# Performance work log

Hardware: AMD Instinct MI355X
Metric: run time of the kernel (lower is better)

## Reference

```python
import jax, jax.numpy as jnp
import numpy as np
from jax import lax

M, T, D, E, NTAGS = 512, 512, 128, 512, 74
GH = D // 2   # GRU hidden per direction (64)
LH = E // 2   # LSTM hidden per direction (256)


def _gru_dir(x, Wih, Whh, bih, bhh):
    # x: [T, Din] -> [T, H]; PyTorch gate order r, z, n
    h = Whh.shape[1]
    gi = x @ Wih.T + bih  # [T, 3H] precomputed input projections
    def step(hprev, gi_t):
        gh = hprev @ Whh.T + bhh
        r = jax.nn.sigmoid(gi_t[:h] + gh[:h])
        z = jax.nn.sigmoid(gi_t[h:2 * h] + gh[h:2 * h])
        n = jnp.tanh(gi_t[2 * h:] + r * gh[2 * h:])
        hnew = (1.0 - z) * n + z * hprev
        return hnew, hnew
    _, hs = lax.scan(step, jnp.zeros((h,), x.dtype), gi)
    return hs


def _bigru(x, Wf, Uf, bf, cf, Wb, Ub, bb, cb):
    hf = _gru_dir(x, Wf, Uf, bf, cf)
    hb = _gru_dir(x[::-1], Wb, Ub, bb, cb)[::-1]
    return jnp.concatenate([hf, hb], axis=-1)


def _lstm_dir(x, Wih, Whh, bih, bhh):
    # PyTorch gate order i, f, g, o
    h = Whh.shape[1]
    gi = x @ Wih.T + bih  # [T, 4H]
    def step(carry, gi_t):
        hprev, cprev = carry
        g = gi_t + hprev @ Whh.T + bhh
        i = jax.nn.sigmoid(g[:h])
        f = jax.nn.sigmoid(g[h:2 * h])
        gg = jnp.tanh(g[2 * h:3 * h])
        o = jax.nn.sigmoid(g[3 * h:])
        c = f * cprev + i * gg
        hnew = o * jnp.tanh(c)
        return (hnew, c), hnew
    init = (jnp.zeros((h,), x.dtype), jnp.zeros((h,), x.dtype))
    _, hs = lax.scan(step, init, gi)
    return hs


def _bilstm(x, Wf, Uf, bf, cf, Wb, Ub, bb, cb):
    hf = _lstm_dir(x, Wf, Uf, bf, cf)
    hb = _lstm_dir(x[::-1], Wb, Ub, bb, cb)[::-1]
    return jnp.concatenate([hf, hb], axis=-1)


def setup_inputs() -> dict:
    key = jax.random.key(0)
    ks = jax.random.split(key, 32)
    s = 0.05
    def n(k, shape, scale=s):
        return jax.random.normal(k, shape, jnp.float32) * scale
    inp = {
        'memory': jax.random.normal(ks[0], (M, T, D), jnp.float32),
        'u': jax.random.normal(ks[1], (T, D), jnp.float32),
        'embed': jax.random.normal(ks[2], (T, E), jnp.float32),
        'W_ff': n(ks[3], (D, 2 * D)), 'b_ff': n(ks[4], (D,)),
        'gWih_f': n(ks[5], (3 * GH, D)), 'gWhh_f': n(ks[6], (3 * GH, GH)),
        'gbih_f': n(ks[7], (3 * GH,)), 'gbhh_f': n(ks[8], (3 * GH,)),
        'gWih_b': n(ks[9], (3 * GH, D)), 'gWhh_b': n(ks[10], (3 * GH, GH)),
        'gbih_b': n(ks[11], (3 * GH,)), 'gbhh_b': n(ks[12], (3 * GH,)),
        'W_k': n(ks[13], (E, D)), 'b_k': n(ks[14], (E,)),
        'lWih_f': n(ks[15], (4 * LH, E)), 'lWhh_f': n(ks[16], (4 * LH, LH)),
        'lbih_f': n(ks[17], (4 * LH,)), 'lbhh_f': n(ks[18], (4 * LH,)),
        'lWih_b': n(ks[19], (4 * LH, E)), 'lWhh_b': n(ks[20], (4 * LH, LH)),
        'lbih_b': n(ks[21], (4 * LH,)), 'lbhh_b': n(ks[22], (4 * LH,)),
        'W_out': n(ks[23], (NTAGS, E)), 'b_out': n(ks[24], (NTAGS,)),
    }
    return inp


def reference(memory, u, embed, W_ff, b_ff,
              gWih_f, gWhh_f, gbih_f, gbhh_f,
              gWih_b, gWhh_b, gbih_b, gbhh_b,
              W_k, b_k,
              lWih_f, lWhh_f, lbih_f, lbhh_f,
              lWih_b, lWhh_b, lbih_b, lbhh_b,
              W_out, b_out):
    # --- memory attention (original: python loop over self._memory) ---
    # p[i] = <flatten(memory[i]), flatten(u)>; softmax over memories
    p = jax.nn.softmax(jnp.einsum('mtd,td->m', memory, u))  # [M]
    cat = jnp.concatenate([memory, jnp.broadcast_to(u, memory.shape)], axis=-1)  # [M,T,2D]
    g = cat @ W_ff.T + b_ff  # [M,T,D] (ff_layer applied per memory)
    G = jnp.einsum('m,mtd->td', p, g)  # weighted sum over memories [T,D]
    # --- session encoder (bidirectional GRU) ---
    h = _bigru(G, gWih_f, gWhh_f, gbih_f, gbhh_f, gWib := gWih_b, gWhh_b, gbih_b, gbhh_b)  # [T,D]
    # --- knowledge encoder ---
    o = (u + h) @ W_k.T + b_k  # [T,E]
    # --- tagging head: BiLSTM over embed + o, then linear + softmax ---
    x = embed + o
    comb = _bilstm(x, lWih_f, lWhh_f, lbih_f, lbhh_f, lWih_b, lWhh_b, lbih_b, lbhh_b)  # [T,E]
    logits = comb @ W_out.T + b_out  # [T, NTAGS]
    return jax.nn.softmax(logits, axis=-1)
```

## Files before the change

### kernel.cpp

```cpp
#include <hip/hip_runtime.h>
#include <math.h>

#define TT 512
#define DD 128
#define MM 512
#define EE 512
#define NTAGS 74
#define GH 64
#define LH 256

typedef _Float16 half_t;
typedef _Float16 v2h __attribute__((ext_vector_type(2)));
typedef _Float16 v8h __attribute__((ext_vector_type(8)));
typedef _Float16 v16h __attribute__((ext_vector_type(16)));
typedef int v4i __attribute__((ext_vector_type(4)));

__device__ __forceinline__ float fdot2f(v2h a, v2h b, float c) {
#if __has_builtin(__builtin_amdgcn_fdot2)
    return __builtin_amdgcn_fdot2(a, b, c, false);
#else
    return c + (float)a[0] * (float)b[0] + (float)a[1] * (float)b[1];
#endif
}

__device__ __forceinline__ int sdot4(int a, int b, int c) {
#if __has_builtin(__builtin_amdgcn_sdot4)
    return __builtin_amdgcn_sdot4(a, b, c, false);
#else
    return c + ((a << 24) >> 24) * ((b << 24) >> 24)
             + ((a << 16) >> 24) * ((b << 16) >> 24)
             + ((a << 8) >> 24) * ((b << 8) >> 24)
             + (a >> 24) * (b >> 24);
#endif
}

__device__ __forceinline__ float sigf(float x) { return 1.f / (1.f + __expf(-x)); }
__device__ __forceinline__ float tanhfast(float x) { return 1.f - 2.f / (__expf(2.f * x) + 1.f); }

__device__ __forceinline__ void lds_barrier() {
    __builtin_amdgcn_sched_barrier(0);
    asm volatile("s_waitcnt lgkmcnt(0)" ::: "memory");
    __builtin_amdgcn_s_barrier();
    __builtin_amdgcn_sched_barrier(0);
}

__device__ __forceinline__ v16h load16(const float* p) {
    float4 x0 = ((const float4*)p)[0];
    float4 x1 = ((const float4*)p)[1];
    float4 x2 = ((const float4*)p)[2];
    float4 x3 = ((const float4*)p)[3];
    v16h r;
    r[0] = (half_t)x0.x; r[1] = (half_t)x0.y; r[2] = (half_t)x0.z; r[3] = (half_t)x0.w;
    r[4] = (half_t)x1.x; r[5] = (half_t)x1.y; r[6] = (half_t)x1.z; r[7] = (half_t)x1.w;
    r[8] = (half_t)x2.x; r[9] = (half_t)x2.y; r[10] = (half_t)x2.z; r[11] = (half_t)x2.w;
    r[12] = (half_t)x3.x; r[13] = (half_t)x3.y; r[14] = (half_t)x3.z; r[15] = (half_t)x3.w;
    return r;
}

#define OPAQUE4(a, b, c, d) \
    asm volatile("" : "+v"(a), "+v"(b), "+v"(c), "+v"(d))
#define OPAQUE6(a, b, c, d, e, f) \
    asm volatile("" : "+v"(a), "+v"(b), "+v"(c), "+v"(d), "+v"(e), "+v"(f))

__device__ __forceinline__ void dot16(const v16h& w, const v8h& h0, const v8h& h1,
                                      float& x0, float& x1) {
    x0 = fdot2f(v2h{w[0], w[1]}, v2h{h0[0], h0[1]}, x0);
    x1 = fdot2f(v2h{w[2], w[3]}, v2h{h0[2], h0[3]}, x1);
    x0 = fdot2f(v2h{w[4], w[5]}, v2h{h0[4], h0[5]}, x0);
    x1 = fdot2f(v2h{w[6], w[7]}, v2h{h0[6], h0[7]}, x1);
    x0 = fdot2f(v2h{w[8], w[9]}, v2h{h1[0], h1[1]}, x0);
    x1 = fdot2f(v2h{w[10], w[11]}, v2h{h1[2], h1[3]}, x1);
    x0 = fdot2f(v2h{w[12], w[13]}, v2h{h1[4], h1[5]}, x0);
    x1 = fdot2f(v2h{w[14], w[15]}, v2h{h1[6], h1[7]}, x1);
}

__device__ __forceinline__ int pack4(int b0, int b1, int b2, int b3) {
    return (b0 & 0xff) | ((b1 & 0xff) << 8) | ((b2 & 0xff) << 16) | (b3 << 24);
}

__device__ __forceinline__ v4i quant16(const float* p, float inv_s) {
    float4 x0 = ((const float4*)p)[0];
    float4 x1 = ((const float4*)p)[1];
    float4 x2 = ((const float4*)p)[2];
    float4 x3 = ((const float4*)p)[3];
    v4i r;
    r.x = pack4(__float2int_rn(x0.x * inv_s), __float2int_rn(x0.y * inv_s),
                __float2int_rn(x0.z * inv_s), __float2int_rn(x0.w * inv_s));
    r.y = pack4(__float2int_rn(x1.x * inv_s), __float2int_rn(x1.y * inv_s),
                __float2int_rn(x1.z * inv_s), __float2int_rn(x1.w * inv_s));
    r.z = pack4(__float2int_rn(x2.x * inv_s), __float2int_rn(x2.y * inv_s),
                __float2int_rn(x2.z * inv_s), __float2int_rn(x2.w * inv_s));
    r.w = pack4(__float2int_rn(x3.x * inv_s), __float2int_rn(x3.y * inv_s),
                __float2int_rn(x3.z * inv_s), __float2int_rn(x3.w * inv_s));
    return r;
}

__global__ __launch_bounds__(256) void k_dots(const float* __restrict__ mem,
                                              const float* __restrict__ u,
                                              float* __restrict__ dots) {
    int m = blockIdx.x;
    const float4* m4 = (const float4*)(mem + (size_t)m * TT * DD);
    const float4* u4 = (const float4*)u;
    float acc = 0.f;
#pragma unroll 4
    for (int it = 0; it < (TT * DD / 4) / 256; ++it) {
        int i = it * 256 + threadIdx.x;
        float4 a = m4[i], b = u4[i];
        acc += a.x * b.x + a.y * b.y + a.z * b.z + a.w * b.w;
    }
    for (int off = 32; off; off >>= 1) acc += __shfl_down(acc, off, 64);
    __shared__ float red[4];
    int w = threadIdx.x >> 6, l = threadIdx.x & 63;
    if (l == 0) red[w] = acc;
    __syncthreads();
    if (threadIdx.x == 0) dots[m] = red[0] + red[1] + red[2] + red[3];
}

__global__ __launch_bounds__(512) void k_softmax_p(const float* __restrict__ dots,
                                                   float* __restrict__ p) {
    int tid = threadIdx.x;
    float v = dots[tid];
    float mx = v;
    for (int off = 32; off; off >>= 1) mx = fmaxf(mx, __shfl_down(mx, off, 64));
    __shared__ float red[8];
    __shared__ float bm, bs;
    int w = tid >> 6, l = tid & 63;
    if (l == 0) red[w] = mx;
    __syncthreads();
    if (tid == 0) {
        float t = red[0];
        for (int i = 1; i < 8; ++i) t = fmaxf(t, red[i]);
        bm = t;
    }
    __syncthreads();
    float e = __expf(v - bm);
    float sm = e;
    for (int off = 32; off; off >>= 1) sm += __shfl_down(sm, off, 64);
    if (l == 0) red[w] = sm;
    __syncthreads();
    if (tid == 0) {
        float t = 0.f;
        for (int i = 0; i < 8; ++i) t += red[i];
        bs = t;
    }
    __syncthreads();
    p[tid] = e / bs;
}

__global__ __launch_bounds__(128) void k_wsum(const float* __restrict__ mem,
                                              const float* __restrict__ p,
                                              float* __restrict__ Mbar) {
    __shared__ float pl[MM];
    for (int i = threadIdx.x; i < MM; i += 128) pl[i] = p[i];
    __syncthreads();
    int i4 = blockIdx.x * 128 + threadIdx.x;
    const float4* m4 = (const float4*)mem;
    float4 acc = {0.f, 0.f, 0.f, 0.f};
#pragma unroll 4
    for (int m = 0; m < MM; ++m) {
        float pm = pl[m];
        float4 a = m4[(size_t)m * (TT * DD / 4) + i4];
        acc.x += pm * a.x; acc.y += pm * a.y; acc.z += pm * a.z; acc.w += pm * a.w;
    }
    ((float4*)Mbar)[i4] = acc;
}

__global__ __launch_bounds__(128) void k_G(const float* __restrict__ Mbar,
                                           const float* __restrict__ u,
                                           const float* __restrict__ Wff,
                                           const float* __restrict__ bff,
                                           float* __restrict__ G) {
    int t = blockIdx.x, d = threadIdx.x;
    __shared__ __align__(16) float Ml[DD], ul[DD];
    Ml[d] = Mbar[t * DD + d];
    ul[d] = u[t * DD + d];
    __syncthreads();
    const float* wr = Wff + (size_t)d * 2 * DD;
    float a0 = 0.f, a1 = 0.f;
#pragma unroll 4
    for (int k = 0; k < DD; ++k) {
        a0 += Ml[k] * wr[k];
        a1 += ul[k] * wr[DD + k];
    }
    G[t * DD + d] = a0 + a1 + bff[d];
}

__global__ __launch_bounds__(384) void k_gru_gi(const float* __restrict__ G,
                                                const float* __restrict__ Wf,
                                                const float* __restrict__ bf,
                                                const float* __restrict__ Wb,
                                                const float* __restrict__ bb,
                                                float* __restrict__ gi) {
    int t = blockIdx.x;
    __shared__ __align__(16) float Gl[DD];
    if (threadIdx.x < DD) Gl[threadIdx.x] = G[t * DD + threadIdx.x];
    __syncthreads();
    int r = threadIdx.x;
    const float* w;
    float b;
    float* o;
    if (r < 192) {
        w = Wf + (size_t)r * DD; b = bf[r]; o = gi + ((size_t)0 * TT + t) * 192 + r;
    } else {
        int rr = r - 192;
        w = Wb + (size_t)rr * DD; b = bb[rr]; o = gi + ((size_t)1 * TT + t) * 192 + rr;
    }
    float a0 = 0.f, a1 = 0.f;
#pragma unroll 4
    for (int k = 0; k < DD; k += 2) {
        a0 += Gl[k] * w[k];
        a1 += Gl[k + 1] * w[k + 1];
    }
    *o = a0 + a1 + b;
}

__global__ __launch_bounds__(256) void k_gru_seq(const float* __restrict__ Whh_f,
                                                 const float* __restrict__ bhh_f,
                                                 const float* __restrict__ Whh_b,
                                                 const float* __restrict__ bhh_b,
                                                 const float* __restrict__ gi,
                                                 float* __restrict__ hbuf) {
    int dir = blockIdx.x;
    int tid = threadIdx.x;
    const float* Whh = dir ? Whh_b : Whh_f;
    const float* bhh = dir ? bhh_b : bhh_f;
    v16h w0 = {}, w1 = {}, w2 = {}, w3 = {};
    float bh = 0.f;
    if (tid < 192) {
        const float* wr = Whh + (size_t)tid * 64;
        w0 = load16(wr);
        w1 = load16(wr + 16);
        w2 = load16(wr + 32);
        w3 = load16(wr + 48);
        bh = bhh[tid];
    }
    OPAQUE4(w0, w1, w2, w3);
    __shared__ __align__(16) half_t hl[64];
    __shared__ float pa[192];
    if (tid < 32) ((v2h*)hl)[tid] = v2h{(half_t)0.f, (half_t)0.f};
    float h = 0.f;
    float g_r = 0.f, g_z = 0.f, g_n = 0.f;
    if (tid < 64) {
        int t0 = dir ? (TT - 1) : 0;
        const float* git = gi + ((size_t)dir * TT + t0) * 192;
        g_r = git[tid]; g_z = git[64 + tid]; g_n = git[128 + tid];
    }
    lds_barrier();
    for (int s = 0; s < TT; ++s) {
        int t = dir ? (TT - 1 - s) : s;
        float p_r = 0.f, p_z = 0.f, p_n = 0.f;
        if (tid < 64) {
            int sn = (s + 1 < TT) ? (s + 1) : s;
            int tn = dir ? (TT - 1 - sn) : sn;
            const float* git = gi + ((size_t)dir * TT + tn) * 192;
            p_r = git[tid]; p_z = git[64 + tid]; p_n = git[128 + tid];
        }
        if (tid < 192) {
            float a0 = bh, a1 = 0.f;
            v8h h0, h1;
            h0 = *(const v8h*)(hl + 0);  h1 = *(const v8h*)(hl + 8);
            dot16(w0, h0, h1, a0, a1);
            h0 = *(const v8h*)(hl + 16); h1 = *(const v8h*)(hl + 24);
            dot16(w1, h0, h1, a0, a1);
            h0 = *(const v8h*)(hl + 32); h1 = *(const v8h*)(hl + 40);
            dot16(w2, h0, h1, a0, a1);
            h0 = *(const v8h*)(hl + 48); h1 = *(const v8h*)(hl + 56);
            dot16(w3, h0, h1, a0, a1);
            pa[tid] = a0 + a1;
        }
        lds_barrier();
        if (tid < 64) {
            float r = sigf(g_r + pa[tid]);
            float z = sigf(g_z + pa[64 + tid]);
            float n = tanhfast(g_n + r * pa[128 + tid]);
            h = (1.f - z) * n + z * h;
            hbuf[t * DD + dir * 64 + tid] = h;
            hl[tid] = (half_t)h;
        }
        lds_barrier();
        g_r = p_r; g_z = p_z; g_n = p_n;
    }
}

__global__ __launch_bounds__(512) void k_x(const float* __restrict__ u,
                                           const float* __restrict__ hbuf,
                                           const float* __restrict__ Wk,
                                           const float* __restrict__ bk,
                                           const float* __restrict__ embed,
                                           float* __restrict__ x) {
    int t = blockIdx.x, e = threadIdx.x;
    __shared__ __align__(16) float sl[DD];
    if (e < DD) sl[e] = u[t * DD + e] + hbuf[t * DD + e];
    __syncthreads();
    const float* wr = Wk + (size_t)e * DD;
    float a0 = 0.f, a1 = 0.f;
#pragma unroll 4
    for (int k = 0; k < DD; k += 2) {
        a0 += sl[k] * wr[k];
        a1 += sl[k + 1] * wr[k + 1];
    }
    x[t * EE + e] = embed[t * EE + e] + a0 + a1 + bk[e];
}

__global__ __launch_bounds__(1024) void k_lstm_gi(const float* __restrict__ x,
                                                  const float* __restrict__ Wf,
                                                  const float* __restrict__ bf,
                                                  const float* __restrict__ Wb,
                                                  const float* __restrict__ bb,
                                                  float* __restrict__ gi) {
    int dir = blockIdx.y;
    int t0 = blockIdx.x * 8;
    __shared__ __align__(16) float xl[8 * EE];
    for (int i = threadIdx.x; i < 8 * EE; i += 1024) xl[i] = x[(size_t)t0 * EE + i];
    __syncthreads();
    int r = threadIdx.x;
    const float* W = dir ? Wb : Wf;
    const float* bi = dir ? bb : bf;
    const float* wr = W + (size_t)r * EE;
    float b = bi[r];
    float acc[8];
#pragma unroll
    for (int uu = 0; uu < 8; ++uu) acc[uu] = b;
    for (int k = 0; k < EE; k += 4) {
        float4 wv = *(const float4*)(wr + k);
#pragma unroll
        for (int uu = 0; uu < 8; ++uu) {
            float4 xv = *(const float4*)(&xl[uu * EE + k]);
            acc[uu] += wv.x * xv.x + wv.y * xv.y + wv.z * xv.z + wv.w * xv.w;
        }
    }
#pragma unroll
    for (int uu = 0; uu < 8; ++uu)
        gi[((size_t)dir * TT + (t0 + uu)) * 1024 + r] = acc[uu];
}

__global__ __launch_bounds__(512) void k_lstm_seq(const float* __restrict__ Whh_f,
                                                  const float* __restrict__ bhh_f,
                                                  const float* __restrict__ Whh_b,
                                                  const float* __restrict__ bhh_b,
                                                  const float* __restrict__ gi,
                                                  float* __restrict__ comb) {
    int dir = blockIdx.x;
    int tid = threadIdx.x;
    int u = tid & 255;
    int hi = tid >> 8;
    int r0 = hi * 256 + u;
    int r1 = 512 + hi * 256 + u;
    const float* Whh = dir ? Whh_b : Whh_f;
    const float* bhh = dir ? bhh_b : bhh_f;

    __shared__ __align__(16) int wsl[4][1024][4];
    __shared__ __align__(16) int hq[64];
    __shared__ float pa[1024];

    const float* s0 = Whh + (size_t)r0 * 256;
    const float* s1 = Whh + (size_t)r1 * 256;
    float mx0 = 0.f, mx1 = 0.f;
    for (int k = 0; k < 256; k += 4) {
        float4 a = *(const float4*)(s0 + k);
        float4 b = *(const float4*)(s1 + k);
        mx0 = fmaxf(mx0, fmaxf(fmaxf(fabsf(a.x), fabsf(a.y)), fmaxf(fabsf(a.z), fabsf(a.w))));
        mx1 = fmaxf(mx1, fmaxf(fmaxf(fabsf(b.x), fabsf(b.y)), fmaxf(fabsf(b.z), fabsf(b.w))));
    }
    float inv0 = 127.f / mx0, inv1 = 127.f / mx1;
    float fs0 = mx0 / 16129.f, fs1 = mx1 / 16129.f;

#pragma unroll
    for (int cc = 0; cc < 4; ++cc) {
        *(v4i*)&wsl[cc][r0][0] = quant16(s0 + 192 + 16 * cc, inv0);
        *(v4i*)&wsl[cc][r1][0] = quant16(s1 + 192 + 16 * cc, inv1);
    }
    v4i wa0 = quant16(s0, inv0),        wa1 = quant16(s0 + 16, inv0),
        wa2 = quant16(s0 + 32, inv0),   wa3 = quant16(s0 + 48, inv0),
        wa4 = quant16(s0 + 64, inv0),   wa5 = quant16(s0 + 80, inv0),
        wa6 = quant16(s0 + 96, inv0),   wa7 = quant16(s0 + 112, inv0),
        wa8 = quant16(s0 + 128, inv0),  wa9 = quant16(s0 + 144, inv0),
        wa10 = quant16(s0 + 160, inv0), wa11 = quant16(s0 + 176, inv0);
    v4i wb0 = quant16(s1, inv1),        wb1 = quant16(s1 + 16, inv1),
        wb2 = quant16(s1 + 32, inv1),   wb3 = quant16(s1 + 48, inv1),
        wb4 = quant16(s1 + 64, inv1),   wb5 = quant16(s1 + 80, inv1),
        wb6 = quant16(s1 + 96, inv1),   wb7 = quant16(s1 + 112, inv1),
        wb8 = quant16(s1 + 128, inv1),  wb9 = quant16(s1 + 144, inv1),
        wb10 = quant16(s1 + 160, inv1), wb11 = quant16(s1 + 176, inv1);
    OPAQUE6(wa0, wa1, wa2, wa3, wa4, wa5);
    OPAQUE6(wa6, wa7, wa8, wa9, wa10, wa11);
    OPAQUE6(wb0, wb1, wb2, wb3, wb4, wb5);
    OPAQUE6(wb6, wb7, wb8, wb9, wb10, wb11);
    float bh0 = bhh[r0], bh1 = bhh[r1];
    if (tid < 64) hq[tid] = 0;
    float c_state = 0.f;
    int tfirst = dir ? (TT - 1) : 0;
    float g0v = gi[((size_t)dir * TT + tfirst) * 1024 + r0];
    float g1v = gi[((size_t)dir * TT + tfirst) * 1024 + r1];
    lds_barrier();

    for (int s = 0; s < TT; ++s) {
        int t = dir ? (TT - 1 - s) : s;
        int sn = (s + 1 < TT) ? (s + 1) : s;
        int tn = dir ? (TT - 1 - sn) : sn;
        const float* gnext = gi + ((size_t)dir * TT + tn) * 1024;
        float g0n = gnext[r0], g1n = gnext[r1];
        int a0 = 0, a1 = 0, b0 = 0, b1 = 0;
        const v4i* h4 = (const v4i*)hq;
#define DOTC(c) { v4i h = h4[c];                                     \
        a0 = sdot4(wa##c.x, h.x, a0); a1 = sdot4(wa##c.y, h.y, a1);  \
        a0 = sdot4(wa##c.z, h.z, a0); a1 = sdot4(wa##c.w, h.w, a1);  \
        b0 = sdot4(wb##c.x, h.x, b0); b1 = sdot4(wb##c.y, h.y, b1);  \
        b0 = sdot4(wb##c.z, h.z, b0); b1 = sdot4(wb##c.w, h.w, b1); }
        DOTC(0); DOTC(1); DOTC(2); DOTC(3); DOTC(4); DOTC(5);
        DOTC(6); DOTC(7); DOTC(8); DOTC(9); DOTC(10); DOTC(11);
#undef DOTC
#pragma unroll
        for (int cc = 0; cc < 4; ++cc) {
            v4i h = h4[12 + cc];
            v4i va = *(const v4i*)&wsl[cc][r0][0];
            v4i vb = *(const v4i*)&wsl[cc][r1][0];
            a0 = sdot4(va.x, h.x, a0); a1 = sdot4(va.y, h.y, a1);
            a0 = sdot4(va.z, h.z, a0); a1 = sdot4(va.w, h.w, a1);
            b0 = sdot4(vb.x, h.x, b0); b1 = sdot4(vb.y, h.y, b1);
            b0 = sdot4(vb.z, h.z, b0); b1 = sdot4(vb.w, h.w, b1);
        }
        pa[r0] = (float)(a0 + a1) * fs0 + bh0 + g0v;
        pa[r1] = (float)(b0 + b1) * fs1 + bh1 + g1v;
        lds_barrier();
        if (tid < 256) {
            float iv = sigf(pa[tid]);
            float fv = sigf(pa[256 + tid]);
            float gv = tanhfast(pa[512 + tid]);
            float ov = sigf(pa[768 + tid]);
            c_state = fv * c_state + iv * gv;
            float h = ov * tanhfast(c_state);
            comb[(size_t)t * EE + dir * 256 + tid] = h;
            ((signed char*)hq)[tid] = (signed char)__float2int_rn(h * 127.f);
        }
        lds_barrier();
        g0v = g0n; g1v = g1n;
    }
}

__global__ __launch_bounds__(128) void k_out(const float* __restrict__ comb,
                                             const float* __restrict__ Wout,
                                             const float* __restrict__ bout,
                                             float* __restrict__ out) {
    int t = blockIdx.x;
    __shared__ __align__(16) float cl[EE];
    __shared__ float ll[NTAGS];
    __shared__ float mred, sred;
    for (int i = threadIdx.x; i < EE; i += 128) cl[i] = comb[(size_t)t * EE + i];
    __syncthreads();
    int e = threadIdx.x;
    if (e < NTAGS) {
        const float* wr = Wout + (size_t)e * EE;
        float a0 = 0.f, a1 = 0.f;
#pragma unroll 4
        for (int k = 0; k < EE; k += 2) {
            a0 += cl[k] * wr[k];
            a1 += cl[k + 1] * wr[k + 1];
        }
        ll[e] = a0 + a1 + bout[e];
    }
    __syncthreads();
    if (threadIdx.x == 0) {
        float m = ll[0];
        for (int i = 1; i < NTAGS; ++i) m = fmaxf(m, ll[i]);
        float ss = 0.f;
        for (int i = 0; i < NTAGS; ++i) ss += __expf(ll[i] - m);
        mred = m;
        sred = ss;
    }
    __syncthreads();
    if (e < NTAGS) out[t * NTAGS + e] = __expf(ll[e] - mred) / sred;
}

#define OFF_DOTS  ((size_t)0)
#define OFF_P     ((size_t)512)
#define OFF_MBAR  ((size_t)1024)
#define OFF_G     ((size_t)66560)
#define OFF_GIG   ((size_t)132096)
#define OFF_HBUF  ((size_t)328704)
#define OFF_X     ((size_t)394240)
#define OFF_GIL   ((size_t)656384)
#define OFF_COMB  ((size_t)1704960)

extern "C" void kernel_launch(void* const* d_in, const int* in_sizes, int n_in,
                              void* d_out, int out_size, void* d_ws, size_t ws_size,
                              hipStream_t stream) {
    const float* memory = (const float*)d_in[0];
    const float* u      = (const float*)d_in[1];
    const float* embed  = (const float*)d_in[2];
    const float* W_ff   = (const float*)d_in[3];
    const float* b_ff   = (const float*)d_in[4];
    const float* gWih_f = (const float*)d_in[5];
    const float* gWhh_f = (const float*)d_in[6];
    const float* gbih_f = (const float*)d_in[7];
    const float* gbhh_f = (const float*)d_in[8];
    const float* gWih_b = (const float*)d_in[9];
    const float* gWhh_b = (const float*)d_in[10];
    const float* gbih_b = (const float*)d_in[11];
    const float* gbhh_b = (const float*)d_in[12];
    const float* W_k    = (const float*)d_in[13];
    const float* b_k    = (const float*)d_in[14];
    const float* lWih_f = (const float*)d_in[15];
    const float* lWhh_f = (const float*)d_in[16];
    const float* lbih_f = (const float*)d_in[17];
    const float* lbhh_f = (const float*)d_in[18];
    const float* lWih_b = (const float*)d_in[19];
    const float* lWhh_b = (const float*)d_in[20];
    const float* lbih_b = (const float*)d_in[21];
    const float* lbhh_b = (const float*)d_in[22];
    const float* W_out  = (const float*)d_in[23];
    const float* b_out  = (const float*)d_in[24];
    float* out = (float*)d_out;
    float* ws = (float*)d_ws;

    float* dots = ws + OFF_DOTS;
    float* p    = ws + OFF_P;
    float* Mbar = ws + OFF_MBAR;
    float* G    = ws + OFF_G;
    float* giG  = ws + OFF_GIG;
    float* hbuf = ws + OFF_HBUF;
    float* x    = ws + OFF_X;
    float* giL  = ws + OFF_GIL;
    float* comb = ws + OFF_COMB;

    k_dots<<<MM, 256, 0, stream>>>(memory, u, dots);
    k_softmax_p<<<1, MM, 0, stream>>>(dots, p);
    k_wsum<<<128, 128, 0, stream>>>(memory, p, Mbar);
    k_G<<<TT, DD, 0, stream>>>(Mbar, u, W_ff, b_ff, G);
    k_gru_gi<<<TT, 384, 0, stream>>>(G, gWih_f, gbih_f, gWih_b, gbih_b, giG);
    k_gru_seq<<<2, 256, 0, stream>>>(gWhh_f, gbhh_f, gWhh_b, gbhh_b, giG, hbuf);
    k_x<<<TT, EE, 0, stream>>>(u, hbuf, W_k, b_k, embed, x);
    k_lstm_gi<<<dim3(64, 2), 1024, 0, stream>>>(x, lWih_f, lbih_f, lWih_b, lbih_b, giL);
    k_lstm_seq<<<2, 512, 0, stream>>>(lWhh_f, lbhh_f, lWhh_b, lbhh_b, giL, comb);
    k_out<<<TT, 128, 0, stream>>>(comb, W_out, b_out, out);
}
```

Measured before the change: 1.343 ms.

## Restructure GRU and LSTM recurrences to keep all gates per thread

The GRU recurrence now runs as a single 64-thread wavefront per direction. Each lane holds all three gate rows of its hidden unit, so the block barriers and the LDS partial-sum exchange become one wave-local LDS fence. The LSTM recurrence now gives each hidden unit a pair of lanes that split the K dimension, hold all four int8-quantized gate rows in registers, and combine partials with a shuffle. This removes the LDS weight spill, the pa buffer and one of the two block barriers per step, and double-buffers the quantized hidden state. The cost is heavier per-thread register and ALU work for each step.

After: 1.332 ms. Within noise of the previous version (-0.8%).

```diff
diff --git a/kernel.cpp b/kernel.cpp
--- a/kernel.cpp
+++ b/kernel.cpp
@@ -41,6 +41,12 @@
     __builtin_amdgcn_sched_barrier(0);
     asm volatile("s_waitcnt lgkmcnt(0)" ::: "memory");
     __builtin_amdgcn_s_barrier();
+    __builtin_amdgcn_sched_barrier(0);
+}
+
+__device__ __forceinline__ void wave_lds_fence() {
+    __builtin_amdgcn_sched_barrier(0);
+    asm volatile("s_waitcnt lgkmcnt(0)" ::: "memory");
     __builtin_amdgcn_sched_barrier(0);
 }
 
@@ -59,8 +65,6 @@
 
 #define OPAQUE4(a, b, c, d) \
     asm volatile("" : "+v"(a), "+v"(b), "+v"(c), "+v"(d))
-#define OPAQUE6(a, b, c, d, e, f) \
-    asm volatile("" : "+v"(a), "+v"(b), "+v"(c), "+v"(d), "+v"(e), "+v"(f))
 
 __device__ __forceinline__ void dot16(const v16h& w, const v8h& h0, const v8h& h1,
                                       float& x0, float& x1) {
@@ -95,6 +99,16 @@
     return r;
 }
 
+__device__ __forceinline__ float rowmax128(const float* p) {
+    float m = 0.f;
+#pragma unroll 8
+    for (int k = 0; k < 128; k += 4) {
+        float4 a = *(const float4*)(p + k);
+        m = fmaxf(m, fmaxf(fmaxf(fabsf(a.x), fabsf(a.y)), fmaxf(fabsf(a.z), fabsf(a.w))));
+    }
+    return m;
+}
+
 __global__ __launch_bounds__(256) void k_dots(const float* __restrict__ mem,
                                               const float* __restrict__ u,
                                               float* __restrict__ dots) {
@@ -214,71 +228,61 @@
     *o = a0 + a1 + b;
 }
 
-__global__ __launch_bounds__(256) void k_gru_seq(const float* __restrict__ Whh_f,
-                                                 const float* __restrict__ bhh_f,
-                                                 const float* __restrict__ Whh_b,
-                                                 const float* __restrict__ bhh_b,
-                                                 const float* __restrict__ gi,
-                                                 float* __restrict__ hbuf) {
+__global__ __launch_bounds__(64) void k_gru_seq(const float* __restrict__ Whh_f,
+                                                const float* __restrict__ bhh_f,
+                                                const float* __restrict__ Whh_b,
+                                                const float* __restrict__ bhh_b,
+                                                const float* __restrict__ gi,
+                                                float* __restrict__ hbuf) {
     int dir = blockIdx.x;
-    int tid = threadIdx.x;
+    int u = threadIdx.x;
     const float* Whh = dir ? Whh_b : Whh_f;
     const float* bhh = dir ? bhh_b : bhh_f;
-    v16h w0 = {}, w1 = {}, w2 = {}, w3 = {};
-    float bh = 0.f;
-    if (tid < 192) {
-        const float* wr = Whh + (size_t)tid * 64;
-        w0 = load16(wr);
-        w1 = load16(wr + 16);
-        w2 = load16(wr + 32);
-        w3 = load16(wr + 48);
-        bh = bhh[tid];
-    }
-    OPAQUE4(w0, w1, w2, w3);
+    const float* wr_ = Whh + (size_t)u * 64;
+    const float* wz_ = Whh + (size_t)(64 + u) * 64;
+    const float* wn_ = Whh + (size_t)(128 + u) * 64;
+    v16h wr0 = load16(wr_), wr1 = load16(wr_ + 16), wr2 = load16(wr_ + 32), wr3 = load16(wr_ + 48);
+    v16h wz0 = load16(wz_), wz1 = load16(wz_ + 16), wz2 = load16(wz_ + 32), wz3 = load16(wz_ + 48);
+    v16h wn0 = load16(wn_), wn1 = load16(wn_ + 16), wn2 = load16(wn_ + 32), wn3 = load16(wn_ + 48);
+    OPAQUE4(wr0, wr1, wr2, wr3);
+    OPAQUE4(wz0, wz1, wz2, wz3);
+    OPAQUE4(wn0, wn1, wn2, wn3);
+    float bh_r = bhh[u], bh_z = bhh[64 + u], bh_n = bhh[128 + u];
+
     __shared__ __align__(16) half_t hl[64];
-    __shared__ float pa[192];
-    if (tid < 32) ((v2h*)hl)[tid] = v2h{(half_t)0.f, (half_t)0.f};
+    hl[u] = (half_t)0.f;
     float h = 0.f;
-    float g_r = 0.f, g_z = 0.f, g_n = 0.f;
-    if (tid < 64) {
-        int t0 = dir ? (TT - 1) : 0;
-        const float* git = gi + ((size_t)dir * TT + t0) * 192;
-        g_r = git[tid]; g_z = git[64 + tid]; g_n = git[128 + tid];
-    }
-    lds_barrier();
+    int t0 = dir ? (TT - 1) : 0;
+    const float* g0p = gi + ((size_t)dir * TT + t0) * 192;
+    float g_r = g0p[u], g_z = g0p[64 + u], g_n = g0p[128 + u];
+    wave_lds_fence();
+
     for (int s = 0; s < TT; ++s) {
         int t = dir ? (TT - 1 - s) : s;
-        float p_r = 0.f, p_z = 0.f, p_n = 0.f;
-        if (tid < 64) {
-            int sn = (s + 1 < TT) ? (s + 1) : s;
-            int tn = dir ? (TT - 1 - sn) : sn;
-            const float* git = gi + ((size_t)dir * TT + tn) * 192;
-            p_r = git[tid]; p_z = git[64 + tid]; p_n = git[128 + tid];
-        }
-        if (tid < 192) {
-            float a0 = bh, a1 = 0.f;
-            v8h h0, h1;
-            h0 = *(const v8h*)(hl + 0);  h1 = *(const v8h*)(hl + 8);
-            dot16(w0, h0, h1, a0, a1);
-            h0 = *(const v8h*)(hl + 16); h1 = *(const v8h*)(hl + 24);
-            dot16(w1, h0, h1, a0, a1);
-            h0 = *(const v8h*)(hl + 32); h1 = *(const v8h*)(hl + 40);
-            dot16(w2, h0, h1, a0, a1);
-            h0 = *(const v8h*)(hl + 48); h1 = *(const v8h*)(hl + 56);
-            dot16(w3, h0, h1, a0, a1);
-            pa[tid] = a0 + a1;
-        }
-        lds_barrier();
-        if (tid < 64) {
-            float r = sigf(g_r + pa[tid]);
-            float z = sigf(g_z + pa[64 + tid]);
-            float n = tanhfast(g_n + r * pa[128 + tid]);
-            h = (1.f - z) * n + z * h;
-            hbuf[t * DD + dir * 64 + tid] = h;
-            hl[tid] = (half_t)h;
-        }
-        lds_barrier();
-        g_r = p_r; g_z = p_z; g_n = p_n;
+        int sn = (s + 1 < TT) ? (s + 1) : s;
+        int tn = dir ? (TT - 1 - sn) : sn;
+        const float* gb = gi + ((size_t)dir * TT + tn) * 192;
+        float pn_r = gb[u], pn_z = gb[64 + u], pn_n = gb[128 + u];
+
+        const v8h* hv = (const v8h*)hl;
+        v8h h0 = hv[0], h1 = hv[1], h2 = hv[2], h3 = hv[3];
+        v8h h4 = hv[4], h5 = hv[5], h6 = hv[6], h7 = hv[7];
+        float ar0 = bh_r, ar1 = 0.f, az0 = bh_z, az1 = 0.f, an0 = bh_n, an1 = 0.f;
+        dot16(wr0, h0, h1, ar0, ar1); dot16(wr1, h2, h3, ar0, ar1);
+        dot16(wr2, h4, h5, ar0, ar1); dot16(wr3, h6, h7, ar0, ar1);
+        dot16(wz0, h0, h1, az0, az1); dot16(wz1, h2, h3, az0, az1);
+        dot16(wz2, h4, h5, az0, az1); dot16(wz3, h6, h7, az0, az1);
+        dot16(wn0, h0, h1, an0, an1); dot16(wn1, h2, h3, an0, an1);
+        dot16(wn2, h4, h5, an0, an1); dot16(wn3, h6, h7, an0, an1);
+
+        float r = sigf(g_r + ar0 + ar1);
+        float z = sigf(g_z + az0 + az1);
+        float n = tanhfast(g_n + r * (an0 + an1));
+        h = (1.f - z) * n + z * h;
+        hbuf[t * DD + dir * 64 + u] = h;
+        hl[u] = (half_t)h;
+        wave_lds_fence();
+        g_r = pn_r; g_z = pn_z; g_n = pn_n;
     }
 }
 
@@ -334,108 +338,98 @@
         gi[((size_t)dir * TT + (t0 + uu)) * 1024 + r] = acc[uu];
 }
 
-__global__ __launch_bounds__(512) void k_lstm_seq(const float* __restrict__ Whh_f,
-                                                  const float* __restrict__ bhh_f,
-                                                  const float* __restrict__ Whh_b,
-                                                  const float* __restrict__ bhh_b,
-                                                  const float* __restrict__ gi,
-                                                  float* __restrict__ comb) {
+__global__ __launch_bounds__(512, 2) void k_lstm_seq(const float* __restrict__ Whh_f,
+                                                     const float* __restrict__ bhh_f,
+                                                     const float* __restrict__ Whh_b,
+                                                     const float* __restrict__ bhh_b,
+                                                     const float* __restrict__ gi,
+                                                     float* __restrict__ comb) {
     int dir = blockIdx.x;
     int tid = threadIdx.x;
-    int u = tid & 255;
-    int hi = tid >> 8;
-    int r0 = hi * 256 + u;
-    int r1 = 512 + hi * 256 + u;
+    int u = tid >> 1;
+    int half = tid & 1;
     const float* Whh = dir ? Whh_b : Whh_f;
     const float* bhh = dir ? bhh_b : bhh_f;
 
-    __shared__ __align__(16) int wsl[4][1024][4];
-    __shared__ __align__(16) int hq[64];
-    __shared__ float pa[1024];
-
-    const float* s0 = Whh + (size_t)r0 * 256;
-    const float* s1 = Whh + (size_t)r1 * 256;
-    float mx0 = 0.f, mx1 = 0.f;
-    for (int k = 0; k < 256; k += 4) {
-        float4 a = *(const float4*)(s0 + k);
-        float4 b = *(const float4*)(s1 + k);
-        mx0 = fmaxf(mx0, fmaxf(fmaxf(fabsf(a.x), fabsf(a.y)), fmaxf(fabsf(a.z), fabsf(a.w))));
-        mx1 = fmaxf(mx1, fmaxf(fmaxf(fabsf(b.x), fabsf(b.y)), fmaxf(fabsf(b.z), fabsf(b.w))));
-    }
-    float inv0 = 127.f / mx0, inv1 = 127.f / mx1;
-    float fs0 = mx0 / 16129.f, fs1 = mx1 / 16129.f;
-
-#pragma unroll
-    for (int cc = 0; cc < 4; ++cc) {
-        *(v4i*)&wsl[cc][r0][0] = quant16(s0 + 192 + 16 * cc, inv0);
-        *(v4i*)&wsl[cc][r1][0] = quant16(s1 + 192 + 16 * cc, inv1);
-    }
-    v4i wa0 = quant16(s0, inv0),        wa1 = quant16(s0 + 16, inv0),
-        wa2 = quant16(s0 + 32, inv0),   wa3 = quant16(s0 + 48, inv0),
-        wa4 = quant16(s0 + 64, inv0),   wa5 = quant16(s0 + 80, inv0),
-        wa6 = quant16(s0 + 96, inv0),   wa7 = quant16(s0 + 112, inv0),
-        wa8 = quant16(s0 + 128, inv0),  wa9 = quant16(s0 + 144, inv0),
-        wa10 = quant16(s0 + 160, inv0), wa11 = quant16(s0 + 176, inv0);
-    v4i wb0 = quant16(s1, inv1),        wb1 = quant16(s1 + 16, inv1),
-        wb2 = quant16(s1 + 32, inv1),   wb3 = quant16(s1 + 48, inv1),
-        wb4 = quant16(s1 + 64, inv1),   wb5 = quant16(s1 + 80, inv1),
-        wb6 = quant16(s1 + 96, inv1),   wb7 = quant16(s1 + 112, inv1),
-        wb8 = quant16(s1 + 128, inv1),  wb9 = quant16(s1 + 144, inv1),
-        wb10 = quant16(s1 + 160, inv1), wb11 = quant16(s1 + 176, inv1);
-    OPAQUE6(wa0, wa1, wa2, wa3, wa4, wa5);
-    OPAQUE6(wa6, wa7, wa8, wa9, wa10, wa11);
-    OPAQUE6(wb0, wb1, wb2, wb3, wb4, wb5);
-    OPAQUE6(wb6, wb7, wb8, wb9, wb10, wb11);
-    float bh0 = bhh[r0], bh1 = bhh[r1];
-    if (tid < 64) hq[tid] = 0;
+    __shared__ __align__(16) int hq[2][64];
+
+    const float* ri = Whh + (size_t)u * 256 + half * 128;
+    const float* rf = Whh + (size_t)(256 + u) * 256 + half * 128;
+    const float* rg = Whh + (size_t)(512 + u) * 256 + half * 128;
+    const float* ro = Whh + (size_t)(768 + u) * 256 + half * 128;
+
+    float mi = rowmax128(ri); mi = fmaxf(mi, __shfl_xor(mi, 1, 64));
+    float mf = rowmax128(rf); mf = fmaxf(mf, __shfl_xor(mf, 1, 64));
+    float mg = rowmax128(rg); mg = fmaxf(mg, __shfl_xor(mg, 1, 64));
+    float mo = rowmax128(ro); mo = fmaxf(mo, __shfl_xor(mo, 1, 64));
+    float inv_i = 127.f / mi, inv_f = 127.f / mf, inv_g = 127.f / mg, inv_o = 127.f / mo;
+    float fs_i = mi / 16129.f, fs_f = mf / 16129.f, fs_g = mg / 16129.f, fs_o = mo / 16129.f;
+
+#define DECLROW(P, ptr, inv)                                                      \
+    v4i P##0 = quant16((ptr), (inv)),       P##1 = quant16((ptr) + 16, (inv)),    \
+        P##2 = quant16((ptr) + 32, (inv)),  P##3 = quant16((ptr) + 48, (inv)),    \
+        P##4 = quant16((ptr) + 64, (inv)),  P##5 = quant16((ptr) + 80, (inv)),    \
+        P##6 = quant16((ptr) + 96, (inv)),  P##7 = quant16((ptr) + 112, (inv));   \
+    OPAQUE4(P##0, P##1, P##2, P##3);                                              \
+    OPAQUE4(P##4, P##5, P##6, P##7)
+
+    DECLROW(wi, ri, inv_i);
+    DECLROW(wf, rf, inv_f);
+    DECLROW(wg, rg, inv_g);
+    DECLROW(wo, ro, inv_o);
+#undef DECLROW
+
+    float bh_i = bhh[u], bh_f = bhh[256 + u], bh_g = bhh[512 + u], bh_o = bhh[768 + u];
+    if (tid < 64) hq[0][tid] = 0;
     float c_state = 0.f;
     int tfirst = dir ? (TT - 1) : 0;
-    float g0v = gi[((size_t)dir * TT + tfirst) * 1024 + r0];
-    float g1v = gi[((size_t)dir * TT + tfirst) * 1024 + r1];
+    const float* gp0 = gi + ((size_t)dir * TT + tfirst) * 1024;
+    float g_i = gp0[u], g_f = gp0[256 + u], g_g = gp0[512 + u], g_o = gp0[768 + u];
     lds_barrier();
+
+#define ROWD1(P, c, A0, A1)                                          \
+    A0 = sdot4(P##c.x, hv##c.x, A0); A1 = sdot4(P##c.y, hv##c.y, A1); \
+    A0 = sdot4(P##c.z, hv##c.z, A0); A1 = sdot4(P##c.w, hv##c.w, A1)
+#define ROWDOT(P, A0, A1)                                                  \
+    ROWD1(P, 0, A0, A1); ROWD1(P, 1, A0, A1); ROWD1(P, 2, A0, A1);         \
+    ROWD1(P, 3, A0, A1); ROWD1(P, 4, A0, A1); ROWD1(P, 5, A0, A1);         \
+    ROWD1(P, 6, A0, A1); ROWD1(P, 7, A0, A1)
 
     for (int s = 0; s < TT; ++s) {
         int t = dir ? (TT - 1 - s) : s;
         int sn = (s + 1 < TT) ? (s + 1) : s;
         int tn = dir ? (TT - 1 - sn) : sn;
-        const float* gnext = gi + ((size_t)dir * TT + tn) * 1024;
-        float g0n = gnext[r0], g1n = gnext[r1];
-        int a0 = 0, a1 = 0, b0 = 0, b1 = 0;
-        const v4i* h4 = (const v4i*)hq;
-#define DOTC(c) { v4i h = h4[c];                                     \
-        a0 = sdot4(wa##c.x, h.x, a0); a1 = sdot4(wa##c.y, h.y, a1);  \
-        a0 = sdot4(wa##c.z, h.z, a0); a1 = sdot4(wa##c.w, h.w, a1);  \
-        b0 = sdot4(wb##c.x, h.x, b0); b1 = sdot4(wb##c.y, h.y, b1);  \
-        b0 = sdot4(wb##c.z, h.z, b0); b1 = sdot4(wb##c.w, h.w, b1); }
-        DOTC(0); DOTC(1); DOTC(2); DOTC(3); DOTC(4); DOTC(5);
-        DOTC(6); DOTC(7); DOTC(8); DOTC(9); DOTC(10); DOTC(11);
-#undef DOTC
-#pragma unroll
-        for (int cc = 0; cc < 4; ++cc) {
-            v4i h = h4[12 + cc];
-            v4i va = *(const v4i*)&wsl[cc][r0][0];
-            v4i vb = *(const v4i*)&wsl[cc][r1][0];
-            a0 = sdot4(va.x, h.x, a0); a1 = sdot4(va.y, h.y, a1);
-            a0 = sdot4(va.z, h.z, a0); a1 = sdot4(va.w, h.w, a1);
-            b0 = sdot4(vb.x, h.x, b0); b1 = sdot4(vb.y, h.y, b1);
-            b0 = sdot4(vb.z, h.z, b0); b1 = sdot4(vb.w, h.w, b1);
-        }
-        pa[r0] = (float)(a0 + a1) * fs0 + bh0 + g0v;
-        pa[r1] = (float)(b0 + b1) * fs1 + bh1 + g1v;
-        lds_barrier();
-        if (tid < 256) {
-            float iv = sigf(pa[tid]);
-            float fv = sigf(pa[256 + tid]);
-            float gv = tanhfast(pa[512 + tid]);
-            float ov = sigf(pa[768 + tid]);
-            c_state = fv * c_state + iv * gv;
-            float h = ov * tanhfast(c_state);
-            comb[(size_t)t * EE + dir * 256 + tid] = h;
-            ((signed char*)hq)[tid] = (signed char)__float2int_rn(h * 127.f);
+        const float* gb = gi + ((size_t)dir * TT + tn) * 1024;
+        float pn_i = gb[u], pn_f = gb[256 + u], pn_g = gb[512 + u], pn_o = gb[768 + u];
+
+        const v4i* hb = (const v4i*)&hq[s & 1][half * 32];
+        v4i hv0 = hb[0], hv1 = hb[1], hv2 = hb[2], hv3 = hb[3];
+        v4i hv4 = hb[4], hv5 = hb[5], hv6 = hb[6], hv7 = hb[7];
+        int ai0 = 0, ai1 = 0, af0 = 0, af1 = 0, ag0 = 0, ag1 = 0, ao0 = 0, ao1 = 0;
+        ROWDOT(wi, ai0, ai1);
+        ROWDOT(wf, af0, af1);
+        ROWDOT(wg, ag0, ag1);
+        ROWDOT(wo, ao0, ao1);
+        int ai = ai0 + ai1; ai += __shfl_xor(ai, 1, 64);
+        int af = af0 + af1; af += __shfl_xor(af, 1, 64);
+        int ag = ag0 + ag1; ag += __shfl_xor(ag, 1, 64);
+        int ao = ao0 + ao1; ao += __shfl_xor(ao, 1, 64);
+
+        float iv = sigf((float)ai * fs_i + bh_i + g_i);
+        float fv = sigf((float)af * fs_f + bh_f + g_f);
+        float gv = tanhfast((float)ag * fs_g + bh_g + g_g);
+        float ov = sigf((float)ao * fs_o + bh_o + g_o);
+        c_state = fv * c_state + iv * gv;
+        float hval = ov * tanhfast(c_state);
+        if (half == 0) {
+            comb[(size_t)t * EE + dir * 256 + u] = hval;
+            ((signed char*)hq[(s + 1) & 1])[u] = (signed char)__float2int_rn(hval * 127.f);
         }
         lds_barrier();
-        g0v = g0n; g1v = g1n;
-    }
+        g_i = pn_i; g_f = pn_f; g_g = pn_g; g_o = pn_o;
+    }
+#undef ROWDOT
+#undef ROWD1
 }
 
 __global__ __launch_bounds__(128) void k_out(const float* __restrict__ comb,
@@ -528,7 +522,7 @@
     k_wsum<<<128, 128, 0, stream>>>(memory, p, Mbar);
     k_G<<<TT, DD, 0, stream>>>(Mbar, u, W_ff, b_ff, G);
     k_gru_gi<<<TT, 384, 0, stream>>>(G, gWih_f, gbih_f, gWih_b, gbih_b, giG);
-    k_gru_seq<<<2, 256, 0, stream>>>(gWhh_f, gbhh_f, gWhh_b, gbhh_b, giG, hbuf);
+    k_gru_seq<<<2, 64, 0, stream>>>(gWhh_f, gbhh_f, gWhh_b, gbhh_b, giG, hbuf);
     k_x<<<TT, EE, 0, stream>>>(u, hbuf, W_k, b_k, embed, x);
     k_lstm_gi<<<dim3(64, 2), 1024, 0, stream>>>(x, lWih_f, lbih_f, lWih_b, lbih_b, giL);
     k_lstm_seq<<<2, 512, 0, stream>>>(lWhh_f, lbhh_f, lWhh_b, lbhh_b, giL, comb);
```
